# Optimization experiments

Hardware: AMD Instinct MI355X
Metric: run time of the kernel (lower is better)

The kernel has to match this reference:

```python
import jax, jax.numpy as jnp
import numpy as np

TAF = 0.05
EPS = 1e-8  # matches torch CosineSimilarity default eps

def _normalize(x):
    # torch cosine sim divides by max(||x||, eps) per vector
    n = jnp.linalg.norm(x, axis=-1, keepdims=True)
    return x / jnp.maximum(n, EPS)

def setup_inputs() -> dict:
    key = jax.random.key(0)
    k1, k2, k3 = jax.random.split(key, 3)
    N, D = 8192, 128
    return {
        "z": jax.random.normal(k1, (N, D), dtype=jnp.float32),
        "z_p": jax.random.normal(k2, (N, D), dtype=jnp.float32),
        "z_n": jax.random.normal(k3, (N, D), dtype=jnp.float32),
    }

def reference(z, z_p, z_n):
    # Fused normalize + matmul instead of broadcasting [N, M, D] intermediates.
    zn = _normalize(z)
    p_sim = zn @ _normalize(z_p).T / TAF   # [N, M]
    n_sim = zn @ _normalize(z_n).T / TAF   # [N, K]
    logits = jnp.concatenate([p_sim, n_sim], axis=1)  # [N, M+K]
    labels = jnp.arange(logits.shape[0])
    logp = jax.nn.log_softmax(logits, axis=-1)
    loss = -jnp.mean(jnp.take_along_axis(logp, labels[:, None], axis=1))
    return loss
```

## Files before the change

kernel.cpp:

```cpp
#include <hip/hip_runtime.h>
#include <hip/hip_bf16.h>
#include <stdint.h>


#define TAF_F 0.05f
constexpr float LOG2E  = 1.4426950408889634f;
constexpr float SCALE  = LOG2E / TAF_F;

constexpr int N_ROWS     = 8192;
constexpr int D_DIM      = 128;
constexpr int TWO_N      = 16384;
constexpr int NJ         = 32;
constexpr int JCHUNK     = TWO_N / NJ;
constexpr int COL_TILE   = 16;
constexpr int NTW        = JCHUNK / COL_TILE;
constexpr int WAVE_ROWS  = 64;
constexpr int ROW_BLOCKS = N_ROWS / WAVE_ROWS;
constexpr int TILE_BYTES = COL_TILE * D_DIM * 2;

typedef __bf16 bf16x8 __attribute__((ext_vector_type(8)));
typedef __bf16 bf16x2 __attribute__((ext_vector_type(2)));
typedef float  f32x4  __attribute__((ext_vector_type(4)));

typedef __attribute__((address_space(3))) uint32_t       lds_u32;
typedef const __attribute__((address_space(1))) uint32_t glb_u32;

#if __has_builtin(__builtin_amdgcn_exp2f)
#define EXP2(x) __builtin_amdgcn_exp2f(x)
#else
#define EXP2(x) exp2f(x)
#endif

__global__ void normalize_diag_kernel(const float* __restrict__ z,
                                      const float* __restrict__ zp,
                                      const float* __restrict__ znm,
                                      __bf16* __restrict__ znb,
                                      __bf16* __restrict__ bnb,
                                      float* __restrict__ diag) {
    const int wv   = threadIdx.x >> 6;
    const int lane = threadIdx.x & 63;
    const int i    = blockIdx.x * 4 + wv;

    const float2 vz = *reinterpret_cast<const float2*>(z   + (size_t)i * D_DIM + lane * 2);
    const float2 vp = *reinterpret_cast<const float2*>(zp  + (size_t)i * D_DIM + lane * 2);
    const float2 vn = *reinterpret_cast<const float2*>(znm + (size_t)i * D_DIM + lane * 2);

    float sz  = vz.x * vz.x + vz.y * vz.y;
    float sp  = vp.x * vp.x + vp.y * vp.y;
    float sn  = vn.x * vn.x + vn.y * vn.y;
    float szp = vz.x * vp.x + vz.y * vp.y;
#pragma unroll
    for (int o = 32; o >= 1; o >>= 1) {
        sz  += __shfl_xor(sz, o);
        sp  += __shfl_xor(sp, o);
        sn  += __shfl_xor(sn, o);
        szp += __shfl_xor(szp, o);
    }
    const float rz = SCALE / fmaxf(sqrtf(sz), 1e-8f);
    const float rp = 1.0f / fmaxf(sqrtf(sp), 1e-8f);
    const float rn = 1.0f / fmaxf(sqrtf(sn), 1e-8f);

    bf16x2 oz = { (__bf16)(vz.x * rz), (__bf16)(vz.y * rz) };
    bf16x2 op = { (__bf16)(vp.x * rp), (__bf16)(vp.y * rp) };
    bf16x2 on = { (__bf16)(vn.x * rn), (__bf16)(vn.y * rn) };
    *reinterpret_cast<bf16x2*>(znb + (size_t)i * D_DIM + lane * 2)            = oz;
    *reinterpret_cast<bf16x2*>(bnb + (size_t)i * D_DIM + lane * 2)            = op;
    *reinterpret_cast<bf16x2*>(bnb + (size_t)(N_ROWS + i) * D_DIM + lane * 2) = on;
    if (lane == 0) {
        const float rz0 = 1.0f / fmaxf(sqrtf(sz), 1e-8f);
        diag[i] = szp * rz0 * rp * (1.0f / TAF_F);
    }
}

__global__ __launch_bounds__(64) void partial_lse_kernel(
        const __bf16* __restrict__ znb,
        const __bf16* __restrict__ bnb,
        float* __restrict__ partial) {
    __shared__ __align__(16) unsigned char lds[TILE_BYTES * 2];

    const int lane = threadIdx.x;
    const int l15  = lane & 15;
    const int l4   = lane >> 4;

    const int bid = blockIdx.x;
    const int swz = (bid & 7) * (4096 / 8) + (bid >> 3);
    const int rowBlk = swz & (ROW_BLOCKS - 1);
    const int jChunk = swz >> 7;
    const int rowBase = rowBlk * WAVE_ROWS;
    const int jBase   = jChunk * JCHUNK;

    const unsigned char* srcBase = reinterpret_cast<const unsigned char*>(bnb);

    auto stageTile = [&](int tile, int buf) {
        const unsigned char* srcTile = srcBase + (size_t)(jBase + tile * COL_TILE) * 256;
        unsigned char* ldsw = lds + buf * TILE_BYTES;
#pragma unroll
        for (int it = 0; it < 4; ++it) {
            const int s = it * 64 + lane;
            const int g = s ^ ((s >> 4) & 7);
            __builtin_amdgcn_global_load_lds(
                (glb_u32*)(srcTile + (size_t)g * 16),
                (lds_u32*)(ldsw + s * 16), 16, 0, 0);
        }
    };

    bf16x8 a[4][4];
#pragma unroll
    for (int s = 0; s < 4; ++s)
#pragma unroll
        for (int kk = 0; kk < 4; ++kk) {
            const __bf16* p = znb + (size_t)(rowBase + s * 16 + l15) * D_DIM + kk * 32 + l4 * 8;
            a[s][kk] = *reinterpret_cast<const bf16x8*>(p);
        }

    float sums[4][4];
#pragma unroll
    for (int s = 0; s < 4; ++s)
#pragma unroll
        for (int e = 0; e < 4; ++e) sums[s][e] = 0.0f;

    stageTile(0, 0);

    for (int t = 0; t < NTW; ++t) {
        stageTile((t + 1) & (NTW - 1), (t + 1) & 1);
        asm volatile("s_waitcnt vmcnt(4)" ::: "memory");

        const unsigned char* ldsr = lds + (t & 1) * TILE_BYTES;
        bf16x8 b[4];
#pragma unroll
        for (int kk = 0; kk < 4; ++kk) {
            const int cl = l15 * 16 + kk * 4 + l4;
            const int ca = cl ^ (l15 & 7);
            b[kk] = *reinterpret_cast<const bf16x8*>(ldsr + ca * 16);
        }
#pragma unroll
        for (int s = 0; s < 4; ++s) {
            f32x4 acc = {0.0f, 0.0f, 0.0f, 0.0f};
#pragma unroll
            for (int kk = 0; kk < 4; ++kk)
                acc = __builtin_amdgcn_mfma_f32_16x16x32_bf16(a[s][kk], b[kk], acc, 0, 0, 0);
#pragma unroll
            for (int e = 0; e < 4; ++e)
                sums[s][e] += EXP2(acc[e]);
        }
    }
    asm volatile("s_waitcnt vmcnt(0)" ::: "memory");

#pragma unroll
    for (int s = 0; s < 4; ++s)
#pragma unroll
        for (int e = 0; e < 4; ++e) {
            float v = sums[s][e];
            v += __shfl_xor(v, 1);
            v += __shfl_xor(v, 2);
            v += __shfl_xor(v, 4);
            v += __shfl_xor(v, 8);
            sums[s][e] = v;
        }
    if (l15 == 0) {
#pragma unroll
        for (int s = 0; s < 4; ++s)
#pragma unroll
            for (int e = 0; e < 4; ++e) {
                const int row = rowBase + s * 16 + l4 * 4 + e;
                partial[(size_t)row * NJ + jChunk] = sums[s][e];
            }
    }
}

__global__ void finalize_rows_kernel(const float* __restrict__ partial,
                                     const float* __restrict__ diag,
                                     float* __restrict__ blocksum) {
    const int t = threadIdx.x;
    const int r = blockIdx.x * 256 + t;
    const float4* prow = reinterpret_cast<const float4*>(partial + (size_t)r * NJ);
    float se = 0.0f;
#pragma unroll
    for (int c = 0; c < NJ / 4; ++c) {
        const float4 v = prow[c];
        se += (v.x + v.y) + (v.z + v.w);
    }
    float res = logf(se) - diag[r];
#pragma unroll
    for (int o = 32; o >= 1; o >>= 1) res += __shfl_xor(res, o);
    __shared__ float red[4];
    if ((t & 63) == 0) red[t >> 6] = res;
    __syncthreads();
    if (t == 0) blocksum[blockIdx.x] = red[0] + red[1] + red[2] + red[3];
}

__global__ void final_kernel(const float* __restrict__ blocksum,
                             float* __restrict__ out) {
    const int t = threadIdx.x;
    float v = (t < 32) ? blocksum[t] : 0.0f;
#pragma unroll
    for (int o = 32; o >= 1; o >>= 1) v += __shfl_xor(v, o);
    if (t == 0) out[0] = v * (1.0f / (float)N_ROWS);
}

extern "C" void kernel_launch(void* const* d_in, const int* in_sizes, int n_in,
                              void* d_out, int out_size, void* d_ws, size_t ws_size,
                              hipStream_t stream) {
    const float* z   = (const float*)d_in[0];
    const float* zp  = (const float*)d_in[1];
    const float* znm = (const float*)d_in[2];

    char* ws = (char*)d_ws;
    __bf16* znb     = (__bf16*)(ws);
    __bf16* bnb     = (__bf16*)(ws + 2097152);
    float*  diag    = (float*)(ws + 6291456);
    float*  partial = (float*)(ws + 6324224);
    float*  blocksum= (float*)(ws + 7372800);
    float*  out     = (float*)d_out;

    normalize_diag_kernel<<<N_ROWS / 4, 256, 0, stream>>>(z, zp, znm, znb, bnb, diag);
    partial_lse_kernel<<<ROW_BLOCKS * NJ, 64, 0, stream>>>(znb, bnb, partial);
    finalize_rows_kernel<<<N_ROWS / 256, 256, 0, stream>>>(partial, diag, blocksum);
    final_kernel<<<1, 64, 0, stream>>>(blocksum, out);
}
```

Before: 58.23 us.

## Quantize normalized embeddings to FP8 and use 32x32x16 FP8 MFMA

The normalize kernel now writes e4m3 FP8 bytes through a software converter instead of bf16. The logsumexp kernel switches to 32x32x16 fp8 MFMA tiles with 32-column LDS tiles and a new swizzle. This halves operand bytes and doubles MFMA throughput per instruction. The cost is much lower precision in logits scaled by 1/0.05*log2e, which risks accuracy of the exp-sum, and heavier per-element conversion work in the normalize kernel.

Result: faster. 53.91 us (-7.4%).

```diff
diff --git a/kernel.cpp b/kernel.cpp
--- a/kernel.cpp
+++ b/kernel.cpp
@@ -12,15 +12,14 @@
 constexpr int TWO_N      = 16384;
 constexpr int NJ         = 32;
 constexpr int JCHUNK     = TWO_N / NJ;
-constexpr int COL_TILE   = 16;
+constexpr int COL_TILE   = 32;
 constexpr int NTW        = JCHUNK / COL_TILE;
 constexpr int WAVE_ROWS  = 64;
 constexpr int ROW_BLOCKS = N_ROWS / WAVE_ROWS;
-constexpr int TILE_BYTES = COL_TILE * D_DIM * 2;
-
-typedef __bf16 bf16x8 __attribute__((ext_vector_type(8)));
+constexpr int TILE_BYTES = COL_TILE * D_DIM;
+
+typedef float  f32x16 __attribute__((ext_vector_type(16)));
 typedef __bf16 bf16x2 __attribute__((ext_vector_type(2)));
-typedef float  f32x4  __attribute__((ext_vector_type(4)));
 
 typedef __attribute__((address_space(3))) uint32_t       lds_u32;
 typedef const __attribute__((address_space(1))) uint32_t glb_u32;
@@ -31,12 +30,26 @@
 #define EXP2(x) exp2f(x)
 #endif
 
-__global__ void normalize_diag_kernel(const float* __restrict__ z,
-                                      const float* __restrict__ zp,
-                                      const float* __restrict__ znm,
-                                      __bf16* __restrict__ znb,
-                                      __bf16* __restrict__ bnb,
-                                      float* __restrict__ diag) {
+__device__ inline unsigned char f32_to_e4m3(float f) {
+    unsigned u = __float_as_uint(f);
+    unsigned sg = (u >> 24) & 0x80u;
+    unsigned au = u & 0x7FFFFFFFu;
+    if (au < 0x3C800000u) return (unsigned char)sg;
+    if (au > 0x43E00000u) au = 0x43E00000u;
+    const unsigned lsb = (au >> 20) & 1u;
+    au += 0x0007FFFFu + lsb;
+    int e = (int)(au >> 23) - 127 + 7;
+    unsigned m = (au >> 20) & 7u;
+    if (e > 15) { e = 15; m = 6u; }
+    return (unsigned char)(sg | ((unsigned)e << 3) | m);
+}
+
+__global__ void normalize_quant_kernel(const float* __restrict__ z,
+                                       const float* __restrict__ zp,
+                                       const float* __restrict__ znm,
+                                       unsigned char* __restrict__ znb8,
+                                       unsigned char* __restrict__ bnb8,
+                                       float* __restrict__ diag) {
     const int wv   = threadIdx.x >> 6;
     const int lane = threadIdx.x & 63;
     const int i    = blockIdx.x * 4 + wv;
@@ -56,31 +69,32 @@
         sn  += __shfl_xor(sn, o);
         szp += __shfl_xor(szp, o);
     }
-    const float rz = SCALE / fmaxf(sqrtf(sz), 1e-8f);
-    const float rp = 1.0f / fmaxf(sqrtf(sp), 1e-8f);
-    const float rn = 1.0f / fmaxf(sqrtf(sn), 1e-8f);
-
-    bf16x2 oz = { (__bf16)(vz.x * rz), (__bf16)(vz.y * rz) };
-    bf16x2 op = { (__bf16)(vp.x * rp), (__bf16)(vp.y * rp) };
-    bf16x2 on = { (__bf16)(vn.x * rn), (__bf16)(vn.y * rn) };
-    *reinterpret_cast<bf16x2*>(znb + (size_t)i * D_DIM + lane * 2)            = oz;
-    *reinterpret_cast<bf16x2*>(bnb + (size_t)i * D_DIM + lane * 2)            = op;
-    *reinterpret_cast<bf16x2*>(bnb + (size_t)(N_ROWS + i) * D_DIM + lane * 2) = on;
-    if (lane == 0) {
-        const float rz0 = 1.0f / fmaxf(sqrtf(sz), 1e-8f);
-        diag[i] = szp * rz0 * rp * (1.0f / TAF_F);
-    }
+    const float rz0 = 1.0f / fmaxf(sqrtf(sz), 1e-8f);
+    const float rzs = rz0 * SCALE;
+    const float rp  = 1.0f / fmaxf(sqrtf(sp), 1e-8f);
+    const float rn  = 1.0f / fmaxf(sqrtf(sn), 1e-8f);
+
+    const unsigned short za = (unsigned short)f32_to_e4m3(vz.x * rzs)
+                            | ((unsigned short)f32_to_e4m3(vz.y * rzs) << 8);
+    const unsigned short pa = (unsigned short)f32_to_e4m3(vp.x * rp)
+                            | ((unsigned short)f32_to_e4m3(vp.y * rp) << 8);
+    const unsigned short na = (unsigned short)f32_to_e4m3(vn.x * rn)
+                            | ((unsigned short)f32_to_e4m3(vn.y * rn) << 8);
+    *reinterpret_cast<unsigned short*>(znb8 + (size_t)i * D_DIM + lane * 2)            = za;
+    *reinterpret_cast<unsigned short*>(bnb8 + (size_t)i * D_DIM + lane * 2)            = pa;
+    *reinterpret_cast<unsigned short*>(bnb8 + (size_t)(N_ROWS + i) * D_DIM + lane * 2) = na;
+    if (lane == 0) diag[i] = szp * rz0 * rp * (1.0f / TAF_F);
 }
 
 __global__ __launch_bounds__(64) void partial_lse_kernel(
-        const __bf16* __restrict__ znb,
-        const __bf16* __restrict__ bnb,
+        const unsigned char* __restrict__ znb8,
+        const unsigned char* __restrict__ bnb8,
         float* __restrict__ partial) {
     __shared__ __align__(16) unsigned char lds[TILE_BYTES * 2];
 
     const int lane = threadIdx.x;
-    const int l15  = lane & 15;
-    const int l4   = lane >> 4;
+    const int l31  = lane & 31;
+    const int l5   = lane >> 5;
 
     const int bid = blockIdx.x;
     const int swz = (bid & 7) * (4096 / 8) + (bid >> 3);
@@ -89,35 +103,32 @@
     const int rowBase = rowBlk * WAVE_ROWS;
     const int jBase   = jChunk * JCHUNK;
 
-    const unsigned char* srcBase = reinterpret_cast<const unsigned char*>(bnb);
-
     auto stageTile = [&](int tile, int buf) {
-        const unsigned char* srcTile = srcBase + (size_t)(jBase + tile * COL_TILE) * 256;
+        const unsigned char* srcTile = bnb8 + (size_t)(jBase + tile * COL_TILE) * D_DIM;
         unsigned char* ldsw = lds + buf * TILE_BYTES;
 #pragma unroll
         for (int it = 0; it < 4; ++it) {
             const int s = it * 64 + lane;
-            const int g = s ^ ((s >> 4) & 7);
+            const int g = (s & ~7) | ((s & 7) ^ ((s >> 3) & 7));
             __builtin_amdgcn_global_load_lds(
                 (glb_u32*)(srcTile + (size_t)g * 16),
                 (lds_u32*)(ldsw + s * 16), 16, 0, 0);
         }
     };
 
-    bf16x8 a[4][4];
-#pragma unroll
-    for (int s = 0; s < 4; ++s)
-#pragma unroll
-        for (int kk = 0; kk < 4; ++kk) {
-            const __bf16* p = znb + (size_t)(rowBase + s * 16 + l15) * D_DIM + kk * 32 + l4 * 8;
-            a[s][kk] = *reinterpret_cast<const bf16x8*>(p);
-        }
-
-    float sums[4][4];
-#pragma unroll
-    for (int s = 0; s < 4; ++s)
-#pragma unroll
-        for (int e = 0; e < 4; ++e) sums[s][e] = 0.0f;
+    long a[2][8];
+#pragma unroll
+    for (int st = 0; st < 2; ++st)
+#pragma unroll
+        for (int kk = 0; kk < 8; ++kk)
+            a[st][kk] = *reinterpret_cast<const long*>(
+                znb8 + (size_t)(rowBase + st * 32 + l31) * D_DIM + kk * 16 + l5 * 8);
+
+    float sums[2][16];
+#pragma unroll
+    for (int st = 0; st < 2; ++st)
+#pragma unroll
+        for (int e = 0; e < 16; ++e) sums[st][e] = 0.0f;
 
     stageTile(0, 0);
 
@@ -126,44 +137,44 @@
         asm volatile("s_waitcnt vmcnt(4)" ::: "memory");
 
         const unsigned char* ldsr = lds + (t & 1) * TILE_BYTES;
-        bf16x8 b[4];
-#pragma unroll
-        for (int kk = 0; kk < 4; ++kk) {
-            const int cl = l15 * 16 + kk * 4 + l4;
-            const int ca = cl ^ (l15 & 7);
-            b[kk] = *reinterpret_cast<const bf16x8*>(ldsr + ca * 16);
-        }
-#pragma unroll
-        for (int s = 0; s < 4; ++s) {
-            f32x4 acc = {0.0f, 0.0f, 0.0f, 0.0f};
-#pragma unroll
-            for (int kk = 0; kk < 4; ++kk)
-                acc = __builtin_amdgcn_mfma_f32_16x16x32_bf16(a[s][kk], b[kk], acc, 0, 0, 0);
-#pragma unroll
-            for (int e = 0; e < 4; ++e)
-                sums[s][e] += EXP2(acc[e]);
+        long b[8];
+#pragma unroll
+        for (int kk = 0; kk < 8; ++kk) {
+            const int q = kk ^ (l31 & 7);
+            b[kk] = *reinterpret_cast<const long*>(ldsr + l31 * D_DIM + q * 16 + l5 * 8);
+        }
+#pragma unroll
+        for (int st = 0; st < 2; ++st) {
+            f32x16 acc = {};
+#pragma unroll
+            for (int kk = 0; kk < 8; ++kk)
+                acc = __builtin_amdgcn_mfma_f32_32x32x16_fp8_fp8(a[st][kk], b[kk], acc, 0, 0, 0);
+#pragma unroll
+            for (int e = 0; e < 16; ++e)
+                sums[st][e] += EXP2(acc[e]);
         }
     }
     asm volatile("s_waitcnt vmcnt(0)" ::: "memory");
 
 #pragma unroll
-    for (int s = 0; s < 4; ++s)
-#pragma unroll
-        for (int e = 0; e < 4; ++e) {
-            float v = sums[s][e];
+    for (int st = 0; st < 2; ++st)
+#pragma unroll
+        for (int e = 0; e < 16; ++e) {
+            float v = sums[st][e];
             v += __shfl_xor(v, 1);
             v += __shfl_xor(v, 2);
             v += __shfl_xor(v, 4);
             v += __shfl_xor(v, 8);
-            sums[s][e] = v;
-        }
-    if (l15 == 0) {
-#pragma unroll
-        for (int s = 0; s < 4; ++s)
-#pragma unroll
-            for (int e = 0; e < 4; ++e) {
-                const int row = rowBase + s * 16 + l4 * 4 + e;
-                partial[(size_t)row * NJ + jChunk] = sums[s][e];
+            v += __shfl_xor(v, 16);
+            sums[st][e] = v;
+        }
+    if (l31 == 0) {
+#pragma unroll
+        for (int st = 0; st < 2; ++st)
+#pragma unroll
+            for (int e = 0; e < 16; ++e) {
+                const int row = rowBase + st * 32 + (e & 3) + 8 * (e >> 2) + 4 * l5;
+                partial[(size_t)row * NJ + jChunk] = sums[st][e];
             }
     }
 }
@@ -206,15 +217,15 @@
     const float* znm = (const float*)d_in[2];
 
     char* ws = (char*)d_ws;
-    __bf16* znb     = (__bf16*)(ws);
-    __bf16* bnb     = (__bf16*)(ws + 2097152);
-    float*  diag    = (float*)(ws + 6291456);
-    float*  partial = (float*)(ws + 6324224);
-    float*  blocksum= (float*)(ws + 7372800);
-    float*  out     = (float*)d_out;
-
-    normalize_diag_kernel<<<N_ROWS / 4, 256, 0, stream>>>(z, zp, znm, znb, bnb, diag);
-    partial_lse_kernel<<<ROW_BLOCKS * NJ, 64, 0, stream>>>(znb, bnb, partial);
+    unsigned char* znb8 = (unsigned char*)(ws);
+    unsigned char* bnb8 = (unsigned char*)(ws + 1048576);
+    float* diag     = (float*)(ws + 3145728);
+    float* partial  = (float*)(ws + 3178496);
+    float* blocksum = (float*)(ws + 4227072);
+    float* out      = (float*)d_out;
+
+    normalize_quant_kernel<<<N_ROWS / 4, 256, 0, stream>>>(z, zp, znm, znb8, bnb8, diag);
+    partial_lse_kernel<<<ROW_BLOCKS * NJ, 64, 0, stream>>>(znb8, bnb8, partial);
     finalize_rows_kernel<<<N_ROWS / 256, 256, 0, stream>>>(partial, diag, blocksum);
     final_kernel<<<1, 64, 0, stream>>>(blocksum, out);
 }
```
